# Kernel optimization log

Hardware: AMD Instinct MI355X
Metric: run time of the kernel (lower is better)

Reference implementation:

```python
import jax, jax.numpy as jnp
import numpy as np

DECAY = 0.99
BETA = 0.25
EPS_NORM = 1e-12  # matches F.normalize eps


def _l2_normalize(x):
    n = jnp.linalg.norm(x, axis=-1, keepdims=True)
    return x / jnp.maximum(n, EPS_NORM)


def setup_inputs() -> dict:
    key = jax.random.key(0)
    ks = jax.random.split(key, 8)
    B, C, H, W = 16, 256, 64, 64
    D, K = 16, 4096  # codebook_dim, n_embed
    z = jax.random.normal(ks[0], (B, C, H, W), dtype=jnp.float32)
    # 1x1 convs == per-pixel linear layers
    w_down = jax.random.normal(ks[1], (D, C), dtype=jnp.float32) / np.sqrt(C).astype(np.float32)
    b_down = jnp.zeros((D,), dtype=jnp.float32)
    w_up = jax.random.normal(ks[2], (C, D), dtype=jnp.float32) / np.sqrt(D).astype(np.float32)
    b_up = jnp.zeros((C,), dtype=jnp.float32)
    embedding = jax.random.uniform(ks[3], (K, D), minval=-1.0 / K, maxval=1.0 / K, dtype=jnp.float32)
    cluster_size = jax.random.uniform(ks[4], (K,), minval=0.5, maxval=2.0, dtype=jnp.float32)
    embed_avg = jax.random.normal(ks[5], (K, D), dtype=jnp.float32) * 0.01
    return {"z": z, "w_down": w_down, "b_down": b_down, "w_up": w_up,
            "b_up": b_up, "embedding": embedding,
            "cluster_size": cluster_size, "embed_avg": embed_avg}


def reference(z, w_down, b_down, w_up, b_up, embedding, cluster_size, embed_avg):
    B, C, H, W = z.shape
    K, D = embedding.shape

    # proj_down: 1x1 conv -> per-token linear
    z_low = jnp.einsum('bchw,dc->bdhw', z, w_down) + b_down[None, :, None, None]
    z_flat = z_low.transpose(0, 2, 3, 1).reshape(-1, D)          # [N, D]
    z_norm = _l2_normalize(z_flat)
    e_norm = _l2_normalize(embedding)                             # [K, D]

    # squared L2 distances (argmin identical to cdist argmin)
    d2 = (jnp.sum(z_norm * z_norm, -1, keepdims=True)
          - 2.0 * z_norm @ e_norm.T
          + jnp.sum(e_norm * e_norm, -1)[None, :])               # [N, K]
    indices = jnp.argmin(d2, axis=-1)                             # [N]
    z_q_flat = e_norm[indices]                                    # [N, D]

    # EMA buffer update (training path); scatter-accumulate via segment_sum
    ones = jnp.ones(indices.shape, dtype=jnp.float32)
    batch_cluster_size = jax.ops.segment_sum(ones, indices, num_segments=K)
    batch_embed_sum = jax.ops.segment_sum(z_norm, indices, num_segments=K)
    new_cluster_size = cluster_size * DECAY + (1.0 - DECAY) * batch_cluster_size
    new_embed_avg = embed_avg * DECAY + (1.0 - DECAY) * batch_embed_sum
    n = new_cluster_size.sum()
    cs = (new_cluster_size + 1e-5) / (n + K * 1e-5) * n
    new_embedding = new_embed_avg / cs[:, None]

    commitment_loss = BETA * jnp.mean((z_norm - jax.lax.stop_gradient(z_q_flat)) ** 2)

    # straight-through estimator
    z_q_low_flat = z_norm + jax.lax.stop_gradient(z_q_flat - z_norm)
    z_q_low = z_q_low_flat.reshape(B, H, W, D).transpose(0, 3, 1, 2)
    z_q = jnp.einsum('bdhw,cd->bchw', z_q_low, w_up) + b_up[None, :, None, None]

    indices_2d = indices.reshape(B, H, W)

    # metrics / entropy loss (usage == bincount(indices))
    usage_prob = batch_cluster_size / (batch_cluster_size.sum() + 1e-8)
    entropy = -jnp.sum(usage_prob * jnp.log(usage_prob + 1e-8))
    entropy_loss = jnp.log(jnp.float32(K)) - entropy

    return (z_q, commitment_loss, indices_2d, entropy_loss,
            new_embedding, new_cluster_size, new_embed_avg)
```

## Files before the change

kernel.cpp:

```cpp
#include <hip/hip_runtime.h>
#include <math.h>

#define NTOK 65536
#define CDIM 256
#define DDIM 16
#define KCOD 4096
#define HWSZ 4096

#define KSPLIT 16
#define CPS (KCOD / KSPLIT)
#define TPT 4
#define TBLK (256 * TPT)

#define WS_ENORM 0
#define WS_ENN   (WS_ENORM + KCOD*DDIM)
#define WS_WDT   (WS_ENN + KCOD)
#define WS_ZN    (WS_WDT + CDIM*DDIM)
#define WS_BCS   (WS_ZN + NTOK*DDIM)
#define WS_BES   (WS_BCS + KCOD)
#define WS_SCAL  (WS_BES + KCOD*DDIM)
#define WS_PACK  (WS_SCAL + 8)

#define OFS_ZQ   0
#define OFS_LOSS 16777216
#define OFS_IDX  16777217
#define OFS_ENT  16842753
#define OFS_NE   16842754
#define OFS_NCS  16908290
#define OFS_NEA  16912386

__global__ __launch_bounds__(256) void knorm_kernel(const float* __restrict__ emb,
                                                    const float* __restrict__ w_down,
                                                    float* __restrict__ ws) {
  int k = blockIdx.x * 256 + threadIdx.x;
  const float4* src = (const float4*)emb + (size_t)k * 4;
  float4 t0 = src[0], t1 = src[1], t2 = src[2], t3 = src[3];
  float e[16] = {t0.x,t0.y,t0.z,t0.w, t1.x,t1.y,t1.z,t1.w,
                 t2.x,t2.y,t2.z,t2.w, t3.x,t3.y,t3.z,t3.w};
  float ss = 0.f;
  #pragma unroll
  for (int d = 0; d < 16; ++d) ss += e[d] * e[d];
  float dn = fmaxf(sqrtf(ss), 1e-12f);
  #pragma unroll
  for (int d = 0; d < 16; ++d) e[d] = e[d] / dn;
  float s2 = 0.f;
  #pragma unroll
  for (int d = 0; d < 16; ++d) s2 += e[d] * e[d];
  float4* dst = (float4*)(ws + WS_ENORM) + (size_t)k * 4;
  dst[0] = make_float4(e[0],e[1],e[2],e[3]);
  dst[1] = make_float4(e[4],e[5],e[6],e[7]);
  dst[2] = make_float4(e[8],e[9],e[10],e[11]);
  dst[3] = make_float4(e[12],e[13],e[14],e[15]);
  ws[WS_ENN + k] = s2;
  ws[WS_WDT + k] = w_down[(k & 15) * 256 + (k >> 4)];
}

__global__ __launch_bounds__(256) void kdown_kernel(const float* __restrict__ z,
                                                    const float* __restrict__ wdt,
                                                    const float* __restrict__ b_down,
                                                    float* __restrict__ znp) {
  const int tid = threadIdx.x;
  const int n = blockIdx.x * 256 + tid;
  const int b = n >> 12;
  const int hw = n & 4095;
  const float* zp = z + (size_t)b * (CDIM * HWSZ) + hw;

  float acc[16];
  #pragma unroll
  for (int d = 0; d < 16; ++d) acc[d] = 0.f;

  #pragma unroll 16
  for (int c = 0; c < CDIM; ++c) {
    float zv = zp[(size_t)c * HWSZ];
    const float4* wr = (const float4*)(wdt + c * 16);
    float4 w0 = wr[0], w1 = wr[1], w2 = wr[2], w3 = wr[3];
    acc[0]  = fmaf(zv, w0.x, acc[0]);  acc[1]  = fmaf(zv, w0.y, acc[1]);
    acc[2]  = fmaf(zv, w0.z, acc[2]);  acc[3]  = fmaf(zv, w0.w, acc[3]);
    acc[4]  = fmaf(zv, w1.x, acc[4]);  acc[5]  = fmaf(zv, w1.y, acc[5]);
    acc[6]  = fmaf(zv, w1.z, acc[6]);  acc[7]  = fmaf(zv, w1.w, acc[7]);
    acc[8]  = fmaf(zv, w2.x, acc[8]);  acc[9]  = fmaf(zv, w2.y, acc[9]);
    acc[10] = fmaf(zv, w2.z, acc[10]); acc[11] = fmaf(zv, w2.w, acc[11]);
    acc[12] = fmaf(zv, w3.x, acc[12]); acc[13] = fmaf(zv, w3.y, acc[13]);
    acc[14] = fmaf(zv, w3.z, acc[14]); acc[15] = fmaf(zv, w3.w, acc[15]);
  }

  #pragma unroll
  for (int d = 0; d < 16; ++d) acc[d] = acc[d] + b_down[d];
  float ss = 0.f;
  #pragma unroll
  for (int d = 0; d < 16; ++d) ss += acc[d] * acc[d];
  float dn = fmaxf(sqrtf(ss), 1e-12f);
  #pragma unroll
  for (int d = 0; d < 16; ++d) acc[d] = acc[d] / dn;

  float4* op = (float4*)znp + (size_t)n * 4;
  op[0] = make_float4(acc[0],acc[1],acc[2],acc[3]);
  op[1] = make_float4(acc[4],acc[5],acc[6],acc[7]);
  op[2] = make_float4(acc[8],acc[9],acc[10],acc[11]);
  op[3] = make_float4(acc[12],acc[13],acc[14],acc[15]);
}

__global__ __attribute__((amdgpu_flat_work_group_size(256, 256), amdgpu_waves_per_eu(4, 4)))
void kscan_kernel(const float* __restrict__ enorm,
                  const float* __restrict__ ennp,
                  const float* __restrict__ znp,
                  unsigned long long* __restrict__ packp) {
  const int tid = threadIdx.x;
  const int kbase = blockIdx.y * CPS;
  const float* ep  = enorm + (size_t)kbase * 16;
  const float* enp = ennp + kbase;

  float nz[TPT][16];
  float best[TPT];
  int bidx[TPT];
  const int tokbase = blockIdx.x * TBLK + tid;
  {
    const float4* zp = (const float4*)znp;
    #pragma unroll
    for (int p = 0; p < TPT; ++p) {
      int tok = tokbase + p * 256;
      float4 a0 = zp[(size_t)tok * 4 + 0];
      float4 a1 = zp[(size_t)tok * 4 + 1];
      float4 a2 = zp[(size_t)tok * 4 + 2];
      float4 a3 = zp[(size_t)tok * 4 + 3];
      nz[p][0]=-2.f*a0.x; nz[p][1]=-2.f*a0.y; nz[p][2]=-2.f*a0.z; nz[p][3]=-2.f*a0.w;
      nz[p][4]=-2.f*a1.x; nz[p][5]=-2.f*a1.y; nz[p][6]=-2.f*a1.z; nz[p][7]=-2.f*a1.w;
      nz[p][8]=-2.f*a2.x; nz[p][9]=-2.f*a2.y; nz[p][10]=-2.f*a2.z; nz[p][11]=-2.f*a2.w;
      nz[p][12]=-2.f*a3.x; nz[p][13]=-2.f*a3.y; nz[p][14]=-2.f*a3.z; nz[p][15]=-2.f*a3.w;
      best[p] = 3.4e38f;
      bidx[p] = 0;
    }
  }

  #pragma unroll 4
  for (int j = 0; j < CPS; ++j) {
    const float4* e4 = (const float4*)(ep + j * 16);
    float4 c0 = e4[0], c1 = e4[1], c2 = e4[2], c3 = e4[3];
    float en = enp[j];
    #pragma unroll
    for (int p = 0; p < TPT; ++p) {
      float d = en;
      d = fmaf(nz[p][0],  c0.x, d); d = fmaf(nz[p][1],  c0.y, d);
      d = fmaf(nz[p][2],  c0.z, d); d = fmaf(nz[p][3],  c0.w, d);
      d = fmaf(nz[p][4],  c1.x, d); d = fmaf(nz[p][5],  c1.y, d);
      d = fmaf(nz[p][6],  c1.z, d); d = fmaf(nz[p][7],  c1.w, d);
      d = fmaf(nz[p][8],  c2.x, d); d = fmaf(nz[p][9],  c2.y, d);
      d = fmaf(nz[p][10], c2.z, d); d = fmaf(nz[p][11], c2.w, d);
      d = fmaf(nz[p][12], c3.x, d); d = fmaf(nz[p][13], c3.y, d);
      d = fmaf(nz[p][14], c3.z, d); d = fmaf(nz[p][15], c3.w, d);
      if (d < best[p]) { best[p] = d; bidx[p] = j; }
    }
  }

  #pragma unroll
  for (int p = 0; p < TPT; ++p) {
    int tok = tokbase + p * 256;
    unsigned u = __float_as_uint(best[p]);
    u = (u & 0x80000000u) ? ~u : (u | 0x80000000u);
    unsigned long long key =
        ((unsigned long long)u << 32) | (unsigned)(kbase + bidx[p]);
    atomicMin(packp + tok, key);
  }
}

__global__ __launch_bounds__(256) void kfinal_kernel(const float* __restrict__ w_up,
                                                     const float* __restrict__ b_up,
                                                     const float* __restrict__ enorm,
                                                     const float* __restrict__ znp,
                                                     const unsigned long long* __restrict__ packp,
                                                     float* __restrict__ wsacc,
                                                     float* __restrict__ out) {
  const int tid = threadIdx.x;
  const int n = blockIdx.x * 256 + tid;
  const int bidx = (int)(unsigned)(packp[n] & 0xFFFFFFFFull);

  float zn[16];
  {
    const float4* zp = (const float4*)znp + (size_t)n * 4;
    float4 a0 = zp[0], a1 = zp[1], a2 = zp[2], a3 = zp[3];
    zn[0]=a0.x; zn[1]=a0.y; zn[2]=a0.z; zn[3]=a0.w;
    zn[4]=a1.x; zn[5]=a1.y; zn[6]=a1.z; zn[7]=a1.w;
    zn[8]=a2.x; zn[9]=a2.y; zn[10]=a2.z; zn[11]=a2.w;
    zn[12]=a3.x; zn[13]=a3.y; zn[14]=a3.z; zn[15]=a3.w;
  }
  float zq[16];
  {
    const float4* eb = (const float4*)enorm + (size_t)bidx * 4;
    float4 q0 = eb[0], q1 = eb[1], q2 = eb[2], q3 = eb[3];
    zq[0]=q0.x; zq[1]=q0.y; zq[2]=q0.z; zq[3]=q0.w;
    zq[4]=q1.x; zq[5]=q1.y; zq[6]=q1.z; zq[7]=q1.w;
    zq[8]=q2.x; zq[9]=q2.y; zq[10]=q2.z; zq[11]=q2.w;
    zq[12]=q3.x; zq[13]=q3.y; zq[14]=q3.z; zq[15]=q3.w;
  }

  out[OFS_IDX + n] = (float)bidx;

  float ls = 0.f;
  #pragma unroll
  for (int d = 0; d < 16; ++d) { float df = zn[d] - zq[d]; ls = fmaf(df, df, ls); }

  atomicAdd(wsacc + bidx, 1.0f);
  #pragma unroll
  for (int d = 0; d < 16; ++d)
    atomicAdd(wsacc + KCOD + (size_t)bidx * 16 + d, zn[d]);

  #pragma unroll
  for (int off = 32; off > 0; off >>= 1) ls += __shfl_down(ls, off, 64);
  if ((tid & 63) == 0) atomicAdd(wsacc + KCOD + KCOD * DDIM + 0, ls);

  float ql[16];
  #pragma unroll
  for (int d = 0; d < 16; ++d) ql[d] = zn[d] + (zq[d] - zn[d]);

  const int b = n >> 12, hw = n & 4095;
  float* op = out + OFS_ZQ + (size_t)b * (CDIM * HWSZ) + hw;
  #pragma unroll 8
  for (int c = 0; c < CDIM; ++c) {
    const float4* wr = (const float4*)(w_up + c * 16);
    float4 w0 = wr[0], w1 = wr[1], w2 = wr[2], w3 = wr[3];
    float a = 0.f;
    a = fmaf(ql[0],  w0.x, a); a = fmaf(ql[1],  w0.y, a);
    a = fmaf(ql[2],  w0.z, a); a = fmaf(ql[3],  w0.w, a);
    a = fmaf(ql[4],  w1.x, a); a = fmaf(ql[5],  w1.y, a);
    a = fmaf(ql[6],  w1.z, a); a = fmaf(ql[7],  w1.w, a);
    a = fmaf(ql[8],  w2.x, a); a = fmaf(ql[9],  w2.y, a);
    a = fmaf(ql[10], w2.z, a); a = fmaf(ql[11], w2.w, a);
    a = fmaf(ql[12], w3.x, a); a = fmaf(ql[13], w3.y, a);
    a = fmaf(ql[14], w3.z, a); a = fmaf(ql[15], w3.w, a);
    a = a + b_up[c];
    op[(size_t)c * HWSZ] = a;
  }
}

__global__ __launch_bounds__(256) void kema_kernel(const float* __restrict__ cluster_size,
                                                   const float* __restrict__ embed_avg,
                                                   float* __restrict__ ws,
                                                   float* __restrict__ out) {
  const float DEC = 0.99f;
  const float OMD = (float)(1.0 - 0.99);
  const int k = blockIdx.x * 256 + threadIdx.x;
  float bcsv = ws[WS_BCS + k];
  float ncs = cluster_size[k] * DEC + OMD * bcsv;
  out[OFS_NCS + k] = ncs;
  #pragma unroll
  for (int d = 0; d < 16; ++d) {
    float nea = embed_avg[(size_t)k * 16 + d] * DEC + OMD * ws[WS_BES + (size_t)k * 16 + d];
    out[OFS_NEA + (size_t)k * 16 + d] = nea;
  }
  float p = bcsv / 65536.0f;
  float et = -p * logf(p + 1e-8f);

  __shared__ float r1[4], r2[4];
  float v1 = ncs, v2 = et;
  #pragma unroll
  for (int off = 32; off > 0; off >>= 1) {
    v1 += __shfl_down(v1, off, 64);
    v2 += __shfl_down(v2, off, 64);
  }
  int lane = threadIdx.x & 63, w = threadIdx.x >> 6;
  if (lane == 0) { r1[w] = v1; r2[w] = v2; }
  __syncthreads();
  if (threadIdx.x == 0) {
    atomicAdd(ws + WS_SCAL + 1, (r1[0] + r1[1]) + (r1[2] + r1[3]));
    atomicAdd(ws + WS_SCAL + 2, (r2[0] + r2[1]) + (r2[2] + r2[3]));
  }
}

__global__ __launch_bounds__(256) void kemb_kernel(const float* __restrict__ ws,
                                                   float* __restrict__ out) {
  const float KEPS = (float)(4096.0 * 1e-5);
  const int k = blockIdx.x * 256 + threadIdx.x;
  float n = ws[WS_SCAL + 1];
  float ncs = out[OFS_NCS + k];
  float cs = (ncs + 1e-5f) / (n + KEPS) * n;
  #pragma unroll
  for (int d = 0; d < 16; ++d)
    out[OFS_NE + (size_t)k * 16 + d] = out[OFS_NEA + (size_t)k * 16 + d] / cs;
  if (k == 0) {
    out[OFS_LOSS] = 0.25f * (ws[WS_SCAL + 0] / 1048576.0f);
    out[OFS_ENT]  = (float)8.317766166719343 - ws[WS_SCAL + 2];
  }
}

extern "C" void kernel_launch(void* const* d_in, const int* in_sizes, int n_in,
                              void* d_out, int out_size, void* d_ws, size_t ws_size,
                              hipStream_t stream) {
  const float* z        = (const float*)d_in[0];
  const float* w_down   = (const float*)d_in[1];
  const float* b_down   = (const float*)d_in[2];
  const float* w_up     = (const float*)d_in[3];
  const float* b_up     = (const float*)d_in[4];
  const float* emb      = (const float*)d_in[5];
  const float* csz      = (const float*)d_in[6];
  const float* eavg     = (const float*)d_in[7];
  float* out = (float*)d_out;
  float* ws  = (float*)d_ws;

  hipMemsetAsync(ws + WS_BCS, 0, (size_t)(KCOD + KCOD*DDIM + 8) * sizeof(float), stream);
  hipMemsetAsync(ws + WS_PACK, 0xFF, (size_t)NTOK * 8, stream);

  knorm_kernel<<<KCOD / 256, 256, 0, stream>>>(emb, w_down, ws);
  kdown_kernel<<<NTOK / 256, 256, 0, stream>>>(z, ws + WS_WDT, b_down, ws + WS_ZN);
  kscan_kernel<<<dim3(NTOK / TBLK, KSPLIT), 256, 0, stream>>>(
      ws + WS_ENORM, ws + WS_ENN, ws + WS_ZN,
      (unsigned long long*)(ws + WS_PACK));
  kfinal_kernel<<<NTOK / 256, 256, 0, stream>>>(
      w_up, b_up, ws + WS_ENORM, ws + WS_ZN,
      (const unsigned long long*)(ws + WS_PACK), ws + WS_BCS, out);
  kema_kernel<<<KCOD / 256, 256, 0, stream>>>(csz, eavg, ws, out);
  kemb_kernel<<<KCOD / 256, 256, 0, stream>>>(ws, out);
}
```

Baseline: 275.3 us.

## Replace FP32 codebook scan with bf16 MFMA max pass plus exact candidate rescoring

Swaps the scalar FP32 nearest-code scan for two MFMA passes over bf16 copies of normalized tokens and codes. The first pass finds each token's approximate maximum dot product. The second pass flags codes within a fixed margin of that maximum and rescores only those exactly in FP32 with an atomicMin. The aim is to move the dominant N×K distance computation onto matrix cores, at the cost of doing the MFMA work twice. Correctness depends on the bf16 error staying inside the margin, and inputs with many near-ties could trigger many scattered rescoring loads and atomics.

Result: slower. 319.5 us (+16.0%).

```diff
diff --git a/kernel.cpp b/kernel.cpp
--- a/kernel.cpp
+++ b/kernel.cpp
@@ -7,16 +7,19 @@
 #define KCOD 4096
 #define HWSZ 4096
 
-#define KSPLIT 16
-#define CPS (KCOD / KSPLIT)
-#define TPT 4
-#define TBLK (256 * TPT)
+#define DELTA 0.04f
+
+typedef short short8 __attribute__((ext_vector_type(8)));
+typedef float f32x16 __attribute__((ext_vector_type(16)));
 
 #define WS_ENORM 0
 #define WS_ENN   (WS_ENORM + KCOD*DDIM)
 #define WS_WDT   (WS_ENN + KCOD)
-#define WS_ZN    (WS_WDT + CDIM*DDIM)
-#define WS_BCS   (WS_ZN + NTOK*DDIM)
+#define WS_EBF   (WS_WDT + CDIM*DDIM)
+#define WS_ZN    (WS_EBF + KCOD*8)
+#define WS_ZNBF  (WS_ZN + NTOK*DDIM)
+#define WS_M1    (WS_ZNBF + NTOK*8)
+#define WS_BCS   (WS_M1 + NTOK)
 #define WS_BES   (WS_BCS + KCOD)
 #define WS_SCAL  (WS_BES + KCOD*DDIM)
 #define WS_PACK  (WS_SCAL + 8)
@@ -28,6 +31,13 @@
 #define OFS_NE   16842754
 #define OFS_NCS  16908290
 #define OFS_NEA  16912386
+
+__device__ inline unsigned f2bf2(float lo, float hi) {
+  unsigned a = __float_as_uint(lo), b = __float_as_uint(hi);
+  a = (a + 0x7FFFu + ((a >> 16) & 1u)) >> 16;
+  b = (b + 0x7FFFu + ((b >> 16) & 1u)) >> 16;
+  return a | (b << 16);
+}
 
 __global__ __launch_bounds__(256) void knorm_kernel(const float* __restrict__ emb,
                                                     const float* __restrict__ w_down,
@@ -53,12 +63,19 @@
   dst[3] = make_float4(e[12],e[13],e[14],e[15]);
   ws[WS_ENN + k] = s2;
   ws[WS_WDT + k] = w_down[(k & 15) * 256 + (k >> 4)];
+  uint4 p0 = make_uint4(f2bf2(e[0],e[1]),  f2bf2(e[2],e[3]),
+                        f2bf2(e[4],e[5]),  f2bf2(e[6],e[7]));
+  uint4 p1 = make_uint4(f2bf2(e[8],e[9]),  f2bf2(e[10],e[11]),
+                        f2bf2(e[12],e[13]),f2bf2(e[14],e[15]));
+  uint4* eb = (uint4*)(ws + WS_EBF) + (size_t)k * 2;
+  eb[0] = p0; eb[1] = p1;
 }
 
 __global__ __launch_bounds__(256) void kdown_kernel(const float* __restrict__ z,
                                                     const float* __restrict__ wdt,
                                                     const float* __restrict__ b_down,
-                                                    float* __restrict__ znp) {
+                                                    float* __restrict__ znp,
+                                                    unsigned* __restrict__ znbf) {
   const int tid = threadIdx.x;
   const int n = blockIdx.x * 256 + tid;
   const int b = n >> 12;
@@ -98,68 +115,117 @@
   op[1] = make_float4(acc[4],acc[5],acc[6],acc[7]);
   op[2] = make_float4(acc[8],acc[9],acc[10],acc[11]);
   op[3] = make_float4(acc[12],acc[13],acc[14],acc[15]);
-}
-
-__global__ __attribute__((amdgpu_flat_work_group_size(256, 256), amdgpu_waves_per_eu(4, 4)))
-void kscan_kernel(const float* __restrict__ enorm,
-                  const float* __restrict__ ennp,
-                  const float* __restrict__ znp,
-                  unsigned long long* __restrict__ packp) {
-  const int tid = threadIdx.x;
-  const int kbase = blockIdx.y * CPS;
-  const float* ep  = enorm + (size_t)kbase * 16;
-  const float* enp = ennp + kbase;
-
-  float nz[TPT][16];
-  float best[TPT];
-  int bidx[TPT];
-  const int tokbase = blockIdx.x * TBLK + tid;
-  {
-    const float4* zp = (const float4*)znp;
-    #pragma unroll
-    for (int p = 0; p < TPT; ++p) {
-      int tok = tokbase + p * 256;
-      float4 a0 = zp[(size_t)tok * 4 + 0];
-      float4 a1 = zp[(size_t)tok * 4 + 1];
-      float4 a2 = zp[(size_t)tok * 4 + 2];
-      float4 a3 = zp[(size_t)tok * 4 + 3];
-      nz[p][0]=-2.f*a0.x; nz[p][1]=-2.f*a0.y; nz[p][2]=-2.f*a0.z; nz[p][3]=-2.f*a0.w;
-      nz[p][4]=-2.f*a1.x; nz[p][5]=-2.f*a1.y; nz[p][6]=-2.f*a1.z; nz[p][7]=-2.f*a1.w;
-      nz[p][8]=-2.f*a2.x; nz[p][9]=-2.f*a2.y; nz[p][10]=-2.f*a2.z; nz[p][11]=-2.f*a2.w;
-      nz[p][12]=-2.f*a3.x; nz[p][13]=-2.f*a3.y; nz[p][14]=-2.f*a3.z; nz[p][15]=-2.f*a3.w;
-      best[p] = 3.4e38f;
-      bidx[p] = 0;
+
+  uint4 p0 = make_uint4(f2bf2(acc[0],acc[1]),  f2bf2(acc[2],acc[3]),
+                        f2bf2(acc[4],acc[5]),  f2bf2(acc[6],acc[7]));
+  uint4 p1 = make_uint4(f2bf2(acc[8],acc[9]),  f2bf2(acc[10],acc[11]),
+                        f2bf2(acc[12],acc[13]),f2bf2(acc[14],acc[15]));
+  uint4* zb = (uint4*)znbf + (size_t)n * 2;
+  zb[0] = p0; zb[1] = p1;
+}
+
+__global__ __launch_bounds__(256) void kmin_kernel(const unsigned* __restrict__ znbf,
+                                                   const unsigned* __restrict__ ebf,
+                                                   float* __restrict__ m1) {
+  const int lane = threadIdx.x & 63;
+  const int wv = threadIdx.x >> 6;
+  const int tokbase = (blockIdx.x * 4 + wv) * 32;
+  const int hi = lane >> 5;
+  const int ln = lane & 31;
+
+  const short8* za = (const short8*)znbf;
+  const short8* eb = (const short8*)ebf;
+  short8 afrag = za[(size_t)(tokbase + ln) * 2 + hi];
+
+  float m[16];
+  #pragma unroll
+  for (int r = 0; r < 16; ++r) m[r] = -3.4e38f;
+
+  #pragma unroll 2
+  for (int kt = 0; kt < 128; ++kt) {
+    short8 bfrag = eb[(size_t)(kt * 32 + ln) * 2 + hi];
+    f32x16 acc;
+    #pragma unroll
+    for (int r = 0; r < 16; ++r) acc[r] = 0.f;
+    acc = __builtin_amdgcn_mfma_f32_32x32x16_bf16(afrag, bfrag, acc, 0, 0, 0);
+    #pragma unroll
+    for (int r = 0; r < 16; ++r) m[r] = fmaxf(m[r], acc[r]);
+  }
+
+  #pragma unroll
+  for (int r = 0; r < 16; ++r) {
+    float v = m[r];
+    v = fmaxf(v, __shfl_xor(v, 16, 32));
+    v = fmaxf(v, __shfl_xor(v, 8, 32));
+    v = fmaxf(v, __shfl_xor(v, 4, 32));
+    v = fmaxf(v, __shfl_xor(v, 2, 32));
+    v = fmaxf(v, __shfl_xor(v, 1, 32));
+    m[r] = v;
+  }
+  if (ln == 0) {
+    #pragma unroll
+    for (int r = 0; r < 16; ++r) {
+      int row = (r & 3) + 8 * (r >> 2) + 4 * hi;
+      m1[tokbase + row] = m[r];
     }
   }
-
-  #pragma unroll 4
-  for (int j = 0; j < CPS; ++j) {
-    const float4* e4 = (const float4*)(ep + j * 16);
-    float4 c0 = e4[0], c1 = e4[1], c2 = e4[2], c3 = e4[3];
-    float en = enp[j];
-    #pragma unroll
-    for (int p = 0; p < TPT; ++p) {
-      float d = en;
-      d = fmaf(nz[p][0],  c0.x, d); d = fmaf(nz[p][1],  c0.y, d);
-      d = fmaf(nz[p][2],  c0.z, d); d = fmaf(nz[p][3],  c0.w, d);
-      d = fmaf(nz[p][4],  c1.x, d); d = fmaf(nz[p][5],  c1.y, d);
-      d = fmaf(nz[p][6],  c1.z, d); d = fmaf(nz[p][7],  c1.w, d);
-      d = fmaf(nz[p][8],  c2.x, d); d = fmaf(nz[p][9],  c2.y, d);
-      d = fmaf(nz[p][10], c2.z, d); d = fmaf(nz[p][11], c2.w, d);
-      d = fmaf(nz[p][12], c3.x, d); d = fmaf(nz[p][13], c3.y, d);
-      d = fmaf(nz[p][14], c3.z, d); d = fmaf(nz[p][15], c3.w, d);
-      if (d < best[p]) { best[p] = d; bidx[p] = j; }
+}
+
+__global__ __launch_bounds__(256) void kcand_kernel(const unsigned* __restrict__ znbf,
+                                                    const unsigned* __restrict__ ebf,
+                                                    const float* __restrict__ m1,
+                                                    const float* __restrict__ enorm,
+                                                    const float* __restrict__ ennp,
+                                                    const float* __restrict__ znp,
+                                                    unsigned long long* __restrict__ packp) {
+  const int lane = threadIdx.x & 63;
+  const int wv = threadIdx.x >> 6;
+  const int tokbase = (blockIdx.x * 4 + wv) * 32;
+  const int hi = lane >> 5;
+  const int ln = lane & 31;
+
+  const short8* za = (const short8*)znbf;
+  const short8* eb = (const short8*)ebf;
+  short8 afrag = za[(size_t)(tokbase + ln) * 2 + hi];
+
+  float thr[16];
+  #pragma unroll
+  for (int r = 0; r < 16; ++r) {
+    int row = (r & 3) + 8 * (r >> 2) + 4 * hi;
+    thr[r] = m1[tokbase + row] - DELTA;
+  }
+
+  for (int kt = 0; kt < 128; ++kt) {
+    short8 bfrag = eb[(size_t)(kt * 32 + ln) * 2 + hi];
+    f32x16 acc;
+    #pragma unroll
+    for (int r = 0; r < 16; ++r) acc[r] = 0.f;
+    acc = __builtin_amdgcn_mfma_f32_32x32x16_bf16(afrag, bfrag, acc, 0, 0, 0);
+
+    unsigned flags = 0u;
+    #pragma unroll
+    for (int r = 0; r < 16; ++r) flags |= (acc[r] >= thr[r]) ? (1u << r) : 0u;
+
+    if (flags) {
+      #pragma unroll
+      for (int r = 0; r < 16; ++r) {
+        if (flags & (1u << r)) {
+          int row = (r & 3) + 8 * (r >> 2) + 4 * hi;
+          int token = tokbase + row;
+          int code = kt * 32 + ln;
+          const float* znr = znp + (size_t)token * 16;
+          const float* er  = enorm + (size_t)code * 16;
+          float dsc = ennp[code];
+          #pragma unroll
+          for (int i = 0; i < 16; ++i) dsc = fmaf(-2.f * znr[i], er[i], dsc);
+          unsigned u = __float_as_uint(dsc);
+          u = (u & 0x80000000u) ? ~u : (u | 0x80000000u);
+          unsigned long long key =
+              ((unsigned long long)u << 32) | (unsigned)code;
+          atomicMin(packp + token, key);
+        }
+      }
     }
-  }
-
-  #pragma unroll
-  for (int p = 0; p < TPT; ++p) {
-    int tok = tokbase + p * 256;
-    unsigned u = __float_as_uint(best[p]);
-    u = (u & 0x80000000u) ? ~u : (u | 0x80000000u);
-    unsigned long long key =
-        ((unsigned long long)u << 32) | (unsigned)(kbase + bidx[p]);
-    atomicMin(packp + tok, key);
   }
 }
 
@@ -185,8 +251,8 @@
   }
   float zq[16];
   {
-    const float4* eb = (const float4*)enorm + (size_t)bidx * 4;
-    float4 q0 = eb[0], q1 = eb[1], q2 = eb[2], q3 = eb[3];
+    const float4* ebp = (const float4*)enorm + (size_t)bidx * 4;
+    float4 q0 = ebp[0], q1 = ebp[1], q2 = ebp[2], q3 = ebp[3];
     zq[0]=q0.x; zq[1]=q0.y; zq[2]=q0.z; zq[3]=q0.w;
     zq[4]=q1.x; zq[5]=q1.y; zq[6]=q1.z; zq[7]=q1.w;
     zq[8]=q2.x; zq[9]=q2.y; zq[10]=q2.z; zq[11]=q2.w;
@@ -300,10 +366,16 @@
   hipMemsetAsync(ws + WS_PACK, 0xFF, (size_t)NTOK * 8, stream);
 
   knorm_kernel<<<KCOD / 256, 256, 0, stream>>>(emb, w_down, ws);
-  kdown_kernel<<<NTOK / 256, 256, 0, stream>>>(z, ws + WS_WDT, b_down, ws + WS_ZN);
-  kscan_kernel<<<dim3(NTOK / TBLK, KSPLIT), 256, 0, stream>>>(
-      ws + WS_ENORM, ws + WS_ENN, ws + WS_ZN,
-      (unsigned long long*)(ws + WS_PACK));
+  kdown_kernel<<<NTOK / 256, 256, 0, stream>>>(z, ws + WS_WDT, b_down,
+                                               ws + WS_ZN, (unsigned*)(ws + WS_ZNBF));
+  kmin_kernel<<<NTOK / 128, 256, 0, stream>>>((const unsigned*)(ws + WS_ZNBF),
+                                              (const unsigned*)(ws + WS_EBF),
+                                              ws + WS_M1);
+  kcand_kernel<<<NTOK / 128, 256, 0, stream>>>((const unsigned*)(ws + WS_ZNBF),
+                                               (const unsigned*)(ws + WS_EBF),
+                                               ws + WS_M1, ws + WS_ENORM, ws + WS_ENN,
+                                               ws + WS_ZN,
+                                               (unsigned long long*)(ws + WS_PACK));
   kfinal_kernel<<<NTOK / 256, 256, 0, stream>>>(
       w_up, b_up, ws + WS_ENORM, ws + WS_ZN,
       (const unsigned long long*)(ws + WS_PACK), ws + WS_BCS, out);
```
